# Kernel optimization log

Measured on AMD Instinct MI355X. Metric: run time of the kernel, lower is better.

## Reference

```python
import jax, jax.numpy as jnp
import numpy as np

D_STATE = 16
D_CONV = 4


def _diag_perm(H, W):
    perm = []
    for off in range(-(H - 1), W):
        for i in range(H):
            j = i + off
            if 0 <= j < W:
                perm.append(i * W + j)
    perm = np.asarray(perm, dtype=np.int32)
    inv = np.argsort(perm).astype(np.int32)
    return perm, inv


def _mamba_block(x, W_in, conv_w, W_xproj, W_dt, b_dt, A_log, W_outm):
    # x: [B, L, E]; shared-weight SimplifiedMambaBlock, expand=1 -> d_inner = E
    Bsz, L, E = x.shape
    d_inner = W_in.shape[1] // 2
    d_state = W_xproj.shape[1] // 2
    xz = x @ W_in                              # [B, L, 2*d_inner]
    xi, z = xz[..., :d_inner], xz[..., d_inner:]
    # causal depthwise conv1d (padding=d_conv-1, trimmed to L)
    xc = jax.lax.conv_general_dilated(
        xi.transpose(0, 2, 1), conv_w, window_strides=(1,),
        padding=[(conv_w.shape[-1] - 1, 0)], feature_group_count=d_inner,
        dimension_numbers=('NCH', 'OIH', 'NCH'))
    xc = jax.nn.silu(xc.transpose(0, 2, 1))    # [B, L, d_inner]
    dtbc = xc @ W_xproj                        # [B, L, 2*d_state]
    dt = jax.nn.softplus(dtbc[..., :d_state] @ W_dt + b_dt)  # [B, L, d_inner]
    Bc = dtbc[..., d_state:]                   # [B, L, d_state]
    A = -jnp.exp(A_log)                        # [d_inner, d_state]

    def step(h, inp):
        dt_t, B_t, x_t = inp                   # [B,d_inner], [B,d_state], [B,d_inner]
        h = h * jnp.exp(A[None] * dt_t[:, :, None]) + B_t[:, None, :] * x_t[:, :, None]
        return h, h.sum(-1)

    h0 = jnp.zeros((Bsz, d_inner, d_state), x.dtype)
    _, y = jax.lax.scan(step, h0, (dt.transpose(1, 0, 2), Bc.transpose(1, 0, 2), xc.transpose(1, 0, 2)))
    y = y.transpose(1, 0, 2)                   # [B, L, d_inner]
    return (y * jax.nn.silu(z)) @ W_outm


def setup_inputs() -> dict:
    key = jax.random.key(0)
    ks = jax.random.split(key, 16)
    B, H, W, E = 8, 32, 32, 1024
    d_inner, d_state = E, D_STATE
    s = lambda n: 1.0 / np.sqrt(n)
    A = np.tile(np.arange(1, d_state + 1, dtype=np.float32), (d_inner, 1))
    return {
        'vision_features': jax.random.normal(ks[0], (B, H * W, E), jnp.float32),
        'W_input': jax.random.normal(ks[1], (E, E), jnp.float32) * s(E),
        'W_in': jax.random.normal(ks[2], (E, 2 * d_inner), jnp.float32) * s(E),
        'conv_w': jax.random.normal(ks[3], (d_inner, 1, D_CONV), jnp.float32) * s(D_CONV),
        'W_xproj': jax.random.normal(ks[4], (d_inner, 2 * d_state), jnp.float32) * s(d_inner),
        'W_dt': jax.random.normal(ks[5], (d_state, d_inner), jnp.float32) * s(d_state),
        'b_dt': jax.random.normal(ks[6], (d_inner,), jnp.float32) * 0.01,
        'A_log': jnp.asarray(np.log(A)),
        'W_outm': jax.random.normal(ks[7], (d_inner, E), jnp.float32) * s(d_inner),
        'dir_w': jnp.full((4,), 0.25, jnp.float32),
        'ln_g': jnp.ones((E,), jnp.float32),
        'ln_b': jnp.zeros((E,), jnp.float32),
        'W_outproj': jax.random.normal(ks[8], (E, E), jnp.float32) * s(E),
        'Wg1': jax.random.normal(ks[9], (E, E // 4), jnp.float32) * s(E),
        'Wg2': jax.random.normal(ks[10], (E // 4, 1), jnp.float32) * s(E // 4),
        'height': H,
        'width': W,
    }


def reference(vision_features, W_input, W_in, conv_w, W_xproj, W_dt, b_dt, A_log,
              W_outm, dir_w, ln_g, ln_b, W_outproj, Wg1, Wg2, height, width):
    B, N, E = vision_features.shape
    H, Wd = int(height), int(width)
    mamba = lambda t: _mamba_block(t, W_in, conv_w, W_xproj, W_dt, b_dt, A_log, W_outm)
    x = vision_features @ W_input              # [B, N, E]
    x2d = x.reshape(B, H, Wd, E)
    # direction 1: row-major
    out1 = mamba(x)
    # direction 2: flipped both spatial dims
    xf = jnp.flip(x2d, (1, 2)).reshape(B, N, E)
    out2 = jnp.flip(mamba(xf).reshape(B, H, Wd, E), (1, 2)).reshape(B, N, E)
    # direction 3: column-major (transpose)
    xt = x2d.transpose(0, 2, 1, 3).reshape(B, N, E)
    out3 = mamba(xt).reshape(B, Wd, H, E).transpose(0, 2, 1, 3).reshape(B, N, E)
    # direction 4: anti-diagonal scan
    perm, inv = _diag_perm(H, Wd)
    out4 = mamba(x[:, perm])[:, inv]
    fused = dir_w[0] * out1 + dir_w[1] * out2 + dir_w[2] * out3 + dir_w[3] * out4
    mu = fused.mean(-1, keepdims=True)
    var = ((fused - mu) ** 2).mean(-1, keepdims=True)
    fused = (fused - mu) * jax.lax.rsqrt(var + 1e-5) * ln_g + ln_b
    enhanced = fused @ W_outproj
    g = jax.nn.sigmoid(jax.nn.silu(vision_features.mean(1, keepdims=True) @ Wg1) @ Wg2)  # [B,1,1]
    return vision_features + g * enhanced
```

## Files before the change

### kernel.cpp

```cpp
#include <hip/hip_runtime.h>

typedef unsigned short u16;
typedef unsigned int u32;
typedef short v8s __attribute__((ext_vector_type(8)));
typedef float v4f __attribute__((ext_vector_type(4)));
typedef float v2f __attribute__((ext_vector_type(2)));

#define B_SZ 8
#define HH 32
#define WW 32
#define NN 1024
#define M1 (B_SZ * NN)
#define M4 (4 * M1)
#define NCHUNK 16
#define CLEN 64
#define CTB 8

__device__ __forceinline__ float bf2f(u16 u) {
    u32 x = ((u32)u) << 16;
    return __builtin_bit_cast(float, x);
}
__device__ __forceinline__ u16 f2bf(float f) {
    u32 x = __builtin_bit_cast(u32, f);
    x = x + 0x7fffu + ((x >> 16) & 1u);
    return (u16)(x >> 16);
}
__device__ __forceinline__ float rcp_(float x) { return __builtin_amdgcn_rcpf(x); }
__device__ __forceinline__ float sigmoidf_(float x) { return rcp_(1.f + __expf(-x)); }
__device__ __forceinline__ float ldf(const void* p, size_t i, int fin) {
    return fin ? ((const float*)p)[i] : bf2f(((const u16*)p)[i]);
}
__device__ __forceinline__ u16 ldbf(const void* p, size_t i, int fin) {
    return fin ? f2bf(((const float*)p)[i]) : ((const u16*)p)[i];
}
__device__ __forceinline__ void gload_lds16(const u16* g, u16* l) {
    __builtin_amdgcn_global_load_lds(
        (const __attribute__((address_space(1))) unsigned int*)g,
        (__attribute__((address_space(3))) unsigned int*)l, 16, 0, 0);
}
__device__ __forceinline__ int dirmap(int d, int t, const int* __restrict__ perm3) {
    if (d == 0) return t;
    if (d == 1) return (NN - 1) - t;
    if (d == 2) return (t & (HH - 1)) * WW + (t >> 5);
    return perm3[t];
}

__global__ void setup_kernel(const u16* __restrict__ raw, int* __restrict__ flags,
                             int* __restrict__ perm, int* __restrict__ inv) {
    if (blockIdx.x == 0 && threadIdx.x == 0) {
        int ok = 0;
        for (int i = 0; i < 512; i++) {
            int e = (raw[i] >> 7) & 0xFF;
            ok += (e >= 100 && e <= 140) ? 1 : 0;
        }
        flags[0] = (ok < 460) ? 1 : 0;
    }
    int t = blockIdx.x * blockDim.x + threadIdx.x;
    if (t >= NN) return;
    int i = t / WW, j = t % WW;
    int off = j - i;
    int start = 0;
    for (int o = -(HH - 1); o < off; ++o) {
        int lo = (0 > -o) ? 0 : -o;
        int hi = (HH - 1 < WW - 1 - o) ? (HH - 1) : (WW - 1 - o);
        start += (hi - lo + 1);
    }
    int lo0 = (0 > -off) ? 0 : -off;
    int r = start + (i - lo0);
    perm[r] = t;
    inv[t] = r;
}

__global__ __launch_bounds__(256) void convert_bf(const void* __restrict__ src,
                                                  u16* __restrict__ dst,
                                                  const int* __restrict__ flags, int n) {
    int fin = flags[0];
    int i = blockIdx.x * 256 + threadIdx.x;
    if (i < n) dst[i] = ldbf(src, (size_t)i, fin);
}

__global__ __launch_bounds__(256) void zero_f32(float* __restrict__ p, int n) {
    int i = blockIdx.x * 256 + threadIdx.x;
    if (i < n) p[i] = 0.f;
}

__global__ __launch_bounds__(256) void transpose_pad4(
        const void* __restrict__ s0, u16* __restrict__ d0,
        const void* __restrict__ s1, u16* __restrict__ d1,
        const void* __restrict__ s2, u16* __restrict__ d2,
        const void* __restrict__ s3, u16* __restrict__ d3,
        const int* __restrict__ flags) {
    int fin = flags[0];
    const int K = 1024;
    int yb = blockIdx.y;
    const void* src;
    u16* dst;
    int Nsrc, n0;
    if (yb < 64)       { src = s0; dst = d0; Nsrc = 2048; n0 = yb * 32; }
    else if (yb < 66)  { src = s1; dst = d1; Nsrc = 32;   n0 = (yb - 64) * 32; }
    else if (yb < 98)  { src = s2; dst = d2; Nsrc = 1024; n0 = (yb - 66) * 32; }
    else               { src = s3; dst = d3; Nsrc = 1024; n0 = (yb - 98) * 32; }
    __shared__ u16 tile[32][33];
    int k0 = blockIdx.x * 32;
    int tx = threadIdx.x & 31, ty = threadIdx.x >> 5;
#pragma unroll
    for (int i = 0; i < 4; i++) {
        int k = k0 + ty + i * 8, n = n0 + tx;
        tile[ty + i * 8][tx] = (n < Nsrc) ? ldbf(src, (size_t)k * Nsrc + n, fin) : (u16)0;
    }
    __syncthreads();
#pragma unroll
    for (int i = 0; i < 4; i++) {
        int n = n0 + ty + i * 8, k = k0 + tx;
        dst[(size_t)n * K + k] = tile[tx][ty + i * 8];
    }
}

template <int EM, int WI, int WJ>
__global__ __launch_bounds__(256, 4) void gemm128(const u16* __restrict__ A,
                                                  const u16* __restrict__ Bt,
                                                  void* __restrict__ out0,
                                                  void* __restrict__ out1,
                                                  int M, int N, int K,
                                                  const int* __restrict__ flags,
                                                  const void* __restrict__ aux0,
                                                  const float* __restrict__ aux1) {
    constexpr int BM = WI * 32;
    constexpr int BN = WJ * 32;
    int fin = flags[0];
    __shared__ __align__(16) u16 As[BM][64];
    __shared__ __align__(16) u16 Bs[BN][64];
    int tid = threadIdx.x;
    int wave = tid >> 6, lane = tid & 63, quad = lane >> 4, l16 = lane & 15;
    int wm = wave >> 1, wn = wave & 1;
    int m0 = blockIdx.x * BM, n0 = blockIdx.y * BN;
    int r8 = tid >> 3, p8 = tid & 7;
    int sw = (p8 ^ (r8 & 7)) * 8;

    const u16* aBase = A  + (size_t)(m0 + r8) * K + sw;
    const u16* bBase = Bt + (size_t)(n0 + r8) * K + sw;
    size_t rstride = (size_t)32 * K;

    v4f acc[WI][WJ];
#pragma unroll
    for (int i = 0; i < WI; i++)
#pragma unroll
        for (int j = 0; j < WJ; j++) acc[i][j] = (v4f){0.f, 0.f, 0.f, 0.f};

    int seg0 = ((0 + quad) ^ (l16 & 7)) * 8;
    int seg1 = ((4 + quad) ^ (l16 & 7)) * 8;

    for (int k0 = 0; k0 < K; k0 += 64) {
#pragma unroll
        for (int c = 0; c < BM / 32; c++)
            gload_lds16(aBase + (size_t)c * rstride + k0, &As[c * 32 + r8][p8 * 8]);
#pragma unroll
        for (int c = 0; c < BN / 32; c++)
            gload_lds16(bBase + (size_t)c * rstride + k0, &Bs[c * 32 + r8][p8 * 8]);
        __syncthreads();
        v8s af[WI], bf[WJ];
#pragma unroll
        for (int i = 0; i < WI; i++)
            af[i] = *(const v8s*)&As[wm * (WI * 16) + i * 16 + l16][seg0];
#pragma unroll
        for (int j = 0; j < WJ; j++)
            bf[j] = *(const v8s*)&Bs[wn * (WJ * 16) + j * 16 + l16][seg0];
#pragma unroll
        for (int i = 0; i < WI; i++)
#pragma unroll
            for (int j = 0; j < WJ; j++)
                acc[i][j] = __builtin_amdgcn_mfma_f32_16x16x32_bf16(af[i], bf[j],
                                                                    acc[i][j], 0, 0, 0);
#pragma unroll
        for (int i = 0; i < WI; i++)
            af[i] = *(const v8s*)&As[wm * (WI * 16) + i * 16 + l16][seg1];
#pragma unroll
        for (int j = 0; j < WJ; j++)
            bf[j] = *(const v8s*)&Bs[wn * (WJ * 16) + j * 16 + l16][seg1];
#pragma unroll
        for (int i = 0; i < WI; i++)
#pragma unroll
            for (int j = 0; j < WJ; j++)
                acc[i][j] = __builtin_amdgcn_mfma_f32_16x16x32_bf16(af[i], bf[j],
                                                                    acc[i][j], 0, 0, 0);
        __syncthreads();
    }

#pragma unroll
    for (int i = 0; i < WI; i++) {
#pragma unroll
        for (int j = 0; j < WJ; j++) {
#pragma unroll
            for (int rr = 0; rr < 4; rr++) {
                int row = m0 + wm * (WI * 16) + i * 16 + quad * 4 + rr;
                int col = n0 + wn * (WJ * 16) + j * 16 + l16;
                float v = acc[i][j][rr];
                size_t oi = (size_t)row * N + col;
                if (EM == 0) {
                    ((u16*)out0)[oi] = f2bf(v);
                } else if (EM == 1) {
                    if (col < 1024) {
                        ((u16*)out0)[(size_t)row * 1024 + col] = f2bf(v);
                    } else {
                        float sz = v * sigmoidf_(v);
                        ((u16*)out1)[(size_t)row * 1024 + (col - 1024)] = f2bf(sz);
                    }
                } else if (EM == 5) {
                    ((float*)out0)[oi] = v;
                } else {
                    float g = aux1[row >> 10];
                    float res = ldf(aux0, oi, fin) + g * v;
                    if (fin) ((float*)out0)[oi] = res;
                    else ((u16*)out0)[oi] = f2bf(res);
                }
            }
        }
    }
}

__global__ __launch_bounds__(256) void conv_tile(const u16* __restrict__ xi,
                                                 const void* __restrict__ cw,
                                                 u16* __restrict__ xc4,
                                                 const int* __restrict__ flags,
                                                 const int* __restrict__ perm3) {
    int fin = flags[0];
    int gblk = blockIdx.x;
    int d = gblk >> 10, blk = gblk & 1023;
    int b = blk >> 7, tc = blk & 127;
    int t0 = tc * CTB;
    __shared__ u16 rows[CTB + 3][1024];
    __shared__ int sp[CTB + 3];
    if (threadIdx.x < CTB + 3) {
        int tt = t0 - 3 + (int)threadIdx.x;
        sp[threadIdx.x] = (tt >= 0) ? dirmap(d, tt, perm3) : -1;
    }
    __syncthreads();
    for (int i = threadIdx.x; i < (CTB + 3) * 128; i += 256) {
        int r = i >> 7, off = (i & 127) * 8;
        int src = sp[r];
        uint4 v = make_uint4(0, 0, 0, 0);
        if (src >= 0)
            v = *(const uint4*)(xi + ((size_t)(b * 1024 + src)) * 1024 + off);
        *(uint4*)&rows[r][off] = v;
    }
    int e0 = threadIdx.x * 4;
    float w[4][4];
#pragma unroll
    for (int ee = 0; ee < 4; ee++)
#pragma unroll
        for (int k = 0; k < 4; k++)
            w[ee][k] = ldf(cw, (size_t)(e0 + ee) * 4 + k, fin);
    __syncthreads();
    u16* outp = xc4 + (size_t)d * M1 * 1024;
#pragma unroll
    for (int t = 0; t < CTB; t++) {
        float a[4] = {0.f, 0.f, 0.f, 0.f};
#pragma unroll
        for (int k = 0; k < 4; k++) {
            uint2 v = *(const uint2*)&rows[t + k][e0];
            const u16* vs = (const u16*)&v;
#pragma unroll
            for (int ee = 0; ee < 4; ee++)
                a[ee] += w[ee][k] * bf2f(vs[ee]);
        }
        u16 o[4];
#pragma unroll
        for (int ee = 0; ee < 4; ee++) o[ee] = f2bf(a[ee] * sigmoidf_(a[ee]));
        *(uint2*)(outp + ((size_t)(b * 1024 + t0 + t)) * 1024 + e0) = *(const uint2*)o;
    }
}

#define SHUF_LO(q) __builtin_shufflevector(q, q, 0, 1)
#define SHUF_HI(q) __builtin_shufflevector(q, q, 2, 3)
#define SCAN_TLOOP(FASTV)                                                      \
    for (int t = 0; t < CLEN; t++) {                                           \
        float xn = 0.f, zn = 0.f;                                              \
        if (t + 1 < CLEN) {                                                    \
            xn = bf2f(xcyz[ix + 1024]);                                        \
            if (PASS == 3) zn = bf2f(zb[zbase + (size_t)s_perm[t + 1] * 1024]);\
        }                                                                      \
        v4f q0 = *(const v4f*)&sdt[t][0];                                      \
        v4f q1 = *(const v4f*)&sdt[t][4];                                      \
        v4f q2 = *(const v4f*)&sdt[t][8];                                      \
        v4f q3 = *(const v4f*)&sdt[t][12];                                     \
        v2f xpv = {bd, 0.f};                                                   \
        xpv += SHUF_LO(q0) * wdt2[0];                                          \
        xpv += SHUF_HI(q0) * wdt2[1];                                          \
        xpv += SHUF_LO(q1) * wdt2[2];                                          \
        xpv += SHUF_HI(q1) * wdt2[3];                                          \
        xpv += SHUF_LO(q2) * wdt2[4];                                          \
        xpv += SHUF_HI(q2) * wdt2[5];                                          \
        xpv += SHUF_LO(q3) * wdt2[6];                                          \
        xpv += SHUF_HI(q3) * wdt2[7];                                          \
        float xp = xpv.x + xpv.y;                                              \
        float ex = __expf(xp);                                                 \
        v4f r0 = *(const v4f*)&sdt[t][16];                                     \
        v4f r1 = *(const v4f*)&sdt[t][20];                                     \
        v4f r2 = *(const v4f*)&sdt[t][24];                                     \
        v4f r3 = *(const v4f*)&sdt[t][28];                                     \
        v2f bc[8];                                                             \
        bc[0] = SHUF_LO(r0); bc[1] = SHUF_HI(r0);                              \
        bc[2] = SHUF_LO(r1); bc[3] = SHUF_HI(r1);                              \
        bc[4] = SHUF_LO(r2); bc[5] = SHUF_HI(r2);                              \
        bc[6] = SHUF_LO(r3); bc[7] = SHUF_HI(r3);                              \
        v2f acc2 = {0.f, 0.f};                                                 \
        if (FASTV) {                                                           \
            float E = rcp_(1.f + ex);           \
            v2f Ev; Ev.x = E; Ev.y = E * E;                                    \
            v2f Estep; Estep.x = Ev.y; Estep.y = Ev.y;                         \
            _Pragma("unroll")                                                  \
            for (int p = 0; p < 8; p++) {                                      \
                h2[p] = h2[p] * Ev + bc[p] * xv;                               \
                acc2 += h2[p];                                                 \
                Ev *= Estep;                                                   \
            }                                                                  \
            if (PASS == 1) ds *= E;                   \
        } else {                                                               \
            float dtv = (xp > 15.f) ? xp : __logf(1.f + ex);                   \
            _Pragma("unroll")                                                  \
            for (int p = 0; p < 8; p++) {                                      \
                v2f es;                                                        \
                es.x = __expf(Ae2[p].x * dtv);                                 \
                es.y = __expf(Ae2[p].y * dtv);                                 \
                h2[p] = h2[p] * es + bc[p] * xv;                               \
                acc2 += h2[p];                                                 \
            }                                                                  \
            if (PASS == 1) ds += dtv;                                          \
        }                                                                      \
        if (PASS == 3) {                                                       \
            float accv = acc2.x + acc2.y;                                      \
            xcyz[ix] = f2bf(accv * zv * wd);  \
        }                                                                      \
        ix += 1024;                                                            \
        xv = xn;                                                               \
        zv = zn;                                                               \
    }

template <int PASS>
__global__ __launch_bounds__(256) void scan_chunk(const float* __restrict__ dtbc,
                                                  u16* __restrict__ xcyz,
                                                  const u16* __restrict__ zb,
                                                  const void* __restrict__ A_log,
                                                  const void* __restrict__ W_dt,
                                                  const void* __restrict__ b_dt,
                                                  const int* __restrict__ flags,
                                                  float* __restrict__ hend,
                                                  float* __restrict__ dtsum,
                                                  const void* __restrict__ dirw,
                                                  const int* __restrict__ perm3) {
    int fin = flags[0];
    int bid = blockIdx.x;
    int ec = bid & 3, c = (bid >> 2) & (NCHUNK - 1), b = (bid >> 6) & 7, d = bid >> 9;
    int e = ec * 256 + threadIdx.x;
    size_t row0 = (size_t)d * M1 + b * 1024 + c * CLEN;
    size_t cix  = (size_t)d * (8 * NCHUNK) + b * NCHUNK + c;
    __shared__ float sdt[CLEN][32];
    __shared__ int s_perm[CLEN];
    {
        const float* src = dtbc + row0 * 64;
        for (int i = threadIdx.x; i < CLEN * 8; i += 256) {
            int t = i >> 3, f = i & 7;
            *(float4*)&sdt[t][f * 4] = *(const float4*)(src + (size_t)t * 64 + f * 4);
        }
        if (PASS == 3 && threadIdx.x < CLEN)
            s_perm[threadIdx.x] = dirmap(d, c * CLEN + (int)threadIdx.x, perm3);
    }
    v2f Ae2[8], wdt2[8];
    bool fast = true;
#pragma unroll
    for (int p = 0; p < 8; p++) {
        float a0 = -__expf(ldf(A_log, (size_t)e * 16 + 2 * p, fin));
        float a1 = -__expf(ldf(A_log, (size_t)e * 16 + 2 * p + 1, fin));
        Ae2[p].x = a0;
        Ae2[p].y = a1;
        fast = fast && fabsf(a0 + (float)(2 * p + 1)) < 1e-3f * (2 * p + 1)
                    && fabsf(a1 + (float)(2 * p + 2)) < 1e-3f * (2 * p + 2);
    }
#pragma unroll
    for (int p = 0; p < 8; p++) {
        wdt2[p].x = ldf(W_dt, (size_t)(2 * p) * 1024 + e, fin);
        wdt2[p].y = ldf(W_dt, (size_t)(2 * p + 1) * 1024 + e, fin);
    }
    float bd = ldf(b_dt, e, fin);
    float wd = (PASS == 3) ? ldf(dirw, d, fin) : 0.f;
    v2f h2[8];
    if (PASS == 1) {
#pragma unroll
        for (int p = 0; p < 8; p++) h2[p] = (v2f){0.f, 0.f};
    } else {
#pragma unroll
        for (int p = 0; p < 8; p++) {
            h2[p].x = hend[(cix * 16 + 2 * p) * 1024 + e];
            h2[p].y = hend[(cix * 16 + 2 * p + 1) * 1024 + e];
        }
    }
    __syncthreads();
    float ds = fast ? 1.f : 0.f;
    size_t ix = row0 * 1024 + e;
    size_t zbase = (size_t)b * 1024 * 1024 + e;
    float xv = bf2f(xcyz[ix]);
    float zv = (PASS == 3) ? bf2f(zb[zbase + (size_t)s_perm[0] * 1024]) : 0.f;
    if (fast) {
        SCAN_TLOOP(true)
    } else {
        SCAN_TLOOP(false)
    }
    if (PASS == 1) {
#pragma unroll
        for (int p = 0; p < 8; p++) {
            hend[(cix * 16 + 2 * p) * 1024 + e] = h2[p].x;
            hend[(cix * 16 + 2 * p + 1) * 1024 + e] = h2[p].y;
        }
        dtsum[cix * 1024 + e] = ds;
    }
}

__global__ __launch_bounds__(256) void scan_combine2(float* __restrict__ hend,
                                                     const float* __restrict__ dtsum,
                                                     const void* __restrict__ A_log,
                                                     const int* __restrict__ flags) {
    int fin = flags[0];
    int bid = blockIdx.x;
    int ec = bid & 3, s = (bid >> 2) & 15, b = (bid >> 6) & 7, d = bid >> 9;
    int e = ec * 256 + threadIdx.x;
    bool fast = true;
#pragma unroll
    for (int s2 = 0; s2 < 16; s2++) {
        float a = -__expf(ldf(A_log, (size_t)e * 16 + s2, fin));
        fast = fast && fabsf(a + (float)(s2 + 1)) < 1e-3f * (s2 + 1);
    }
    float Ae = -__expf(ldf(A_log, (size_t)e * 16 + s, fin));
    float H = 0.f;
    size_t base = (size_t)d * (8 * NCHUNK) + (size_t)b * NCHUNK;
    for (int c = 0; c < NCHUNK; c++) {
        size_t cix = base + c;
        float ds = dtsum[cix * 1024 + e];
        float decay;
        if (fast) {
            float r = 1.f, bb = ds;
            int n = s + 1;
            while (n) {
                if (n & 1) r *= bb;
                bb *= bb;
                n >>= 1;
            }
            decay = r;
        } else {
            decay = __expf(Ae * ds);
        }
        size_t idx = (cix * 16 + s) * 1024 + e;
        float loc = hend[idx];
        hend[idx] = H;
        H = loc + decay * H;
    }
}

__global__ __launch_bounds__(256) void ln4_kernel(const u16* __restrict__ y4,
                                                  const void* __restrict__ ln_g,
                                                  const void* __restrict__ ln_b,
                                                  const int* __restrict__ flags,
                                                  const int* __restrict__ inv3,
                                                  u16* __restrict__ fn) {
    int fin = flags[0];
    int row = blockIdx.x;
    int b = row >> 10, q = row & 1023;
    int t1 = 1023 - q;
    int t2 = ((q & 31) << 5) | (q >> 5);
    int t3 = inv3[q];
    const u16* p0 = y4 + ((size_t)(b * 1024 + q)) * 1024;
    const u16* p1 = y4 + ((size_t)(M1 + b * 1024 + t1)) * 1024;
    const u16* p2 = y4 + ((size_t)(2 * M1 + b * 1024 + t2)) * 1024;
    const u16* p3 = y4 + ((size_t)(3 * M1 + b * 1024 + t3)) * 1024;
    int e0 = threadIdx.x * 4;
    uint2 a0 = *(const uint2*)(p0 + e0);
    uint2 a1 = *(const uint2*)(p1 + e0);
    uint2 a2 = *(const uint2*)(p2 + e0);
    uint2 a3 = *(const uint2*)(p3 + e0);
    const u16* s0 = (const u16*)&a0;
    const u16* s1 = (const u16*)&a1;
    const u16* s2 = (const u16*)&a2;
    const u16* s3 = (const u16*)&a3;
    float v[4];
    float sum = 0.f, sq = 0.f;
#pragma unroll
    for (int j = 0; j < 4; j++) {
        float f = bf2f(s0[j]) + bf2f(s1[j]) + bf2f(s2[j]) + bf2f(s3[j]);
        v[j] = f;
        sum += f;
        sq += f * f;
    }
    __shared__ float r1[256], r2[256];
    r1[threadIdx.x] = sum;
    r2[threadIdx.x] = sq;
    __syncthreads();
    for (int s = 128; s > 0; s >>= 1) {
        if (threadIdx.x < s) {
            r1[threadIdx.x] += r1[threadIdx.x + s];
            r2[threadIdx.x] += r2[threadIdx.x + s];
        }
        __syncthreads();
    }
    float mu = r1[0] * (1.f / 1024.f);
    float var = r2[0] * (1.f / 1024.f) - mu * mu;
    float rs = rsqrtf(var + 1e-5f);
    u16 o[4];
#pragma unroll
    for (int j = 0; j < 4; j++) {
        int e = e0 + j;
        o[j] = f2bf((v[j] - mu) * rs * ldf(ln_g, e, fin) + ldf(ln_b, e, fin));
    }
    *(uint2*)(fn + (size_t)row * 1024 + e0) = *(const uint2*)o;
}

__global__ __launch_bounds__(256) void gate_partial(const u16* __restrict__ vfb,
                                                    float* __restrict__ meanv) {
    int b = blockIdx.x >> 4, tc = blockIdx.x & 15;
    float s[4] = {0.f, 0.f, 0.f, 0.f};
    const u16* base = vfb + ((size_t)b * 1024 + tc * 64) * 1024;
    for (int t = 0; t < 64; t++) {
#pragma unroll
        for (int k = 0; k < 4; k++)
            s[k] += bf2f(base[(size_t)t * 1024 + threadIdx.x + k * 256]);
    }
#pragma unroll
    for (int k = 0; k < 4; k++)
        atomicAdd(&meanv[b * 1024 + threadIdx.x + k * 256], s[k]);
}

__global__ __launch_bounds__(256) void gate_mv(const float* __restrict__ meanv,
                                               const void* __restrict__ Wg1,
                                               const int* __restrict__ flags,
                                               float* __restrict__ gpart) {
    int fin = flags[0];
    int kc = blockIdx.x, j = threadIdx.x;
    __shared__ float mv[8][32];
    if (threadIdx.x < 8 * 32) {
        int b = threadIdx.x >> 5, kk = threadIdx.x & 31;
        mv[b][kk] = meanv[b * 1024 + kc * 32 + kk] * (1.f / 1024.f);
    }
    __syncthreads();
    float acc[8];
#pragma unroll
    for (int b = 0; b < 8; b++) acc[b] = 0.f;
    for (int kk = 0; kk < 32; kk++) {
        float w = ldf(Wg1, (size_t)(kc * 32 + kk) * 256 + j, fin);
#pragma unroll
        for (int b = 0; b < 8; b++) acc[b] += mv[b][kk] * w;
    }
#pragma unroll
    for (int b = 0; b < 8; b++) atomicAdd(&gpart[b * 256 + j], acc[b]);
}

__global__ __launch_bounds__(256) void gate_fin2(const float* __restrict__ gpart,
                                                 const void* __restrict__ Wg2,
                                                 const int* __restrict__ flags,
                                                 float* __restrict__ g) {
    int fin = flags[0];
    int b = blockIdx.x, j = threadIdx.x;
    __shared__ float red[256];
    float a = gpart[b * 256 + j];
    float si = a * sigmoidf_(a);
    red[j] = si * ldf(Wg2, j, fin);
    __syncthreads();
    for (int st = 128; st > 0; st >>= 1) {
        if (j < st) red[j] += red[j + st];
        __syncthreads();
    }
    if (j == 0) g[b] = sigmoidf_(red[0]);
}

extern "C" void kernel_launch(void* const* d_in, const int* in_sizes, int n_in,
                              void* d_out, int out_size, void* d_ws, size_t ws_size,
                              hipStream_t stream) {
    const void* vf_raw  = d_in[0];
    const void* W_input = d_in[1];
    const void* W_in    = d_in[2];
    const void* conv_w  = d_in[3];
    const void* W_xproj = d_in[4];
    const void* W_dt    = d_in[5];
    const void* b_dt    = d_in[6];
    const void* A_log   = d_in[7];
    const void* W_outm  = d_in[8];
    const void* dir_w   = d_in[9];
    const void* ln_g    = d_in[10];
    const void* ln_b    = d_in[11];
    const void* W_outpj = d_in[12];
    const void* Wg1     = d_in[13];
    const void* Wg2     = d_in[14];

    char* ws = (char*)d_ws;
    size_t off = 0;
    auto alloc = [&](size_t bytes) -> void* {
        void* p = ws + off;
        off = (off + bytes + 255) & ~(size_t)255;
        return p;
    };
    int*   flags = (int*)alloc(256);
    int*   perm3 = (int*)alloc(NN * 4);
    int*   inv3  = (int*)alloc(NN * 4);
    float* meanv = (float*)alloc(8 * 1024 * 4);
    float* gpart = (float*)alloc(8 * 256 * 4);
    float* gbuf  = (float*)alloc(64);
    u16*   WiB   = (u16*)alloc((size_t)1024 * 1024 * 2);
    u16*   WtIn  = (u16*)alloc((size_t)2048 * 1024 * 2);
    u16*   WtF   = (u16*)alloc((size_t)2048 * 1024 * 2);
    u16*   WtXp  = (u16*)alloc((size_t)64 * 1024 * 2);
    u16*   WtOm  = (u16*)alloc((size_t)1024 * 1024 * 2);
    u16*   WtOp  = (u16*)alloc((size_t)1024 * 1024 * 2);
    u16*   vfb   = (u16*)alloc((size_t)M1 * 1024 * 2);
    u16*   xbuf  = (u16*)alloc((size_t)M1 * 1024 * 2);
    float* tail32= (float*)alloc((size_t)M1 * 1024 * 4);
    u16*   xi    = (u16*)alloc((size_t)M1 * 1024 * 2);
    u16*   zb    = (u16*)alloc((size_t)M1 * 1024 * 2);
    u16*   xc4   = (u16*)alloc((size_t)M4 * 1024 * 2);
    float* dtbc4 = (float*)alloc((size_t)M4 * 64 * 4);
    float* dtsum4= (float*)alloc((size_t)4 * 8 * NCHUNK * 1024 * 4);
    float* hend4 = (float*)vfb;
    u16*   y4    = (u16*)vfb;
    (void)tail32;
    (void)xbuf;

    setup_kernel<<<4, 256, 0, stream>>>((const u16*)vf_raw, flags, perm3, inv3);
    convert_bf<<<(M1 * 1024) / 256, 256, 0, stream>>>(vf_raw, vfb, flags, M1 * 1024);
    convert_bf<<<(1024 * 1024) / 256, 256, 0, stream>>>(W_input, WiB, flags, 1024 * 1024);
    transpose_pad4<<<dim3(32, 130), 256, 0, stream>>>(
        W_in, WtIn, W_xproj, WtXp, W_outm, WtOm, W_outpj, WtOp, flags);
    zero_f32<<<40, 256, 0, stream>>>(meanv, 8 * 1024 + 8 * 256);

    gemm128<0, 2, 2><<<dim3(32, 16), 256, 0, stream>>>(
        WtIn, WiB, WtF, nullptr, 2048, 1024, 1024, flags, nullptr, nullptr);

    gate_partial<<<128, 256, 0, stream>>>(vfb, meanv);
    gate_mv<<<32, 256, 0, stream>>>(meanv, Wg1, flags, gpart);
    gate_fin2<<<8, 256, 0, stream>>>(gpart, Wg2, flags, gbuf);

    gemm128<1, 4, 4><<<dim3(64, 16), 256, 0, stream>>>(
        vfb, WtF, xi, zb, M1, 2048, 1024, flags, nullptr, nullptr);

    conv_tile<<<4096, 256, 0, stream>>>(xi, conv_w, xc4, flags, perm3);
    gemm128<5, 2, 2><<<dim3(512, 1), 256, 0, stream>>>(
        xc4, WtXp, dtbc4, nullptr, M4, 64, 1024, flags, nullptr, nullptr);
    scan_chunk<1><<<2048, 256, 0, stream>>>(dtbc4, xc4, zb, A_log, W_dt, b_dt,
                                            flags, hend4, dtsum4, dir_w, perm3);
    scan_combine2<<<2048, 256, 0, stream>>>(hend4, dtsum4, A_log, flags);
    scan_chunk<3><<<2048, 256, 0, stream>>>(dtbc4, xc4, zb, A_log, W_dt, b_dt,
                                            flags, hend4, dtsum4, dir_w, perm3);

    gemm128<0, 4, 4><<<dim3(256, 8), 256, 0, stream>>>(
        xc4, WtOm, y4, nullptr, M4, 1024, 1024, flags, nullptr, nullptr);

    u16* fn = xi;
    ln4_kernel<<<M1, 256, 0, stream>>>(y4, ln_g, ln_b, flags, inv3, fn);
    gemm128<4, 4, 4><<<dim3(64, 8), 256, 0, stream>>>(
        fn, WtOp, d_out, nullptr, M1, 1024, 1024, flags, vf_raw, gbuf);
}
```

Baseline: 615.9 us.

## Process two channels per thread in chunked scan to amortize shared dt/B loads

Each scan_chunk thread now handles two adjacent d_inner channels, reusing the per-timestep shared-memory dt/B reads for both and using packed 32-bit global loads and stores for x, z and y. The grid is halved to match, and launch bounds request 4 blocks per SM. The slow path reloads A_log through volatile loads inside the inner loop to save registers, which would be expensive if that path ran. Doubling per-thread state raises register pressure and halves the number of parallel threads.

```diff
diff --git a/kernel.cpp b/kernel.cpp
--- a/kernel.cpp
+++ b/kernel.cpp
@@ -29,6 +29,10 @@
 __device__ __forceinline__ float sigmoidf_(float x) { return rcp_(1.f + __expf(-x)); }
 __device__ __forceinline__ float ldf(const void* p, size_t i, int fin) {
     return fin ? ((const float*)p)[i] : bf2f(((const u16*)p)[i]);
+}
+__device__ __forceinline__ float ldf_v(const void* p, size_t i, int fin) {
+    return fin ? ((volatile const float*)p)[i]
+               : bf2f(((volatile const u16*)p)[i]);
 }
 __device__ __forceinline__ u16 ldbf(const void* p, size_t i, int fin) {
     return fin ? f2bf(((const float*)p)[i]) : ((const u16*)p)[i];
@@ -274,26 +278,29 @@
 #define SHUF_HI(q) __builtin_shufflevector(q, q, 2, 3)
 #define SCAN_TLOOP(FASTV)                                                      \
     for (int t = 0; t < CLEN; t++) {                                           \
-        float xn = 0.f, zn = 0.f;                                              \
+        u32 xnw = 0, znw = 0;                                                  \
         if (t + 1 < CLEN) {                                                    \
-            xn = bf2f(xcyz[ix + 1024]);                                        \
-            if (PASS == 3) zn = bf2f(zb[zbase + (size_t)s_perm[t + 1] * 1024]);\
+            xnw = *(const u32*)&xcyz[ix + 1024];                               \
+            if (PASS == 3)                                                     \
+                znw = *(const u32*)&zb[zbase + (size_t)s_perm[t + 1] * 1024];  \
         }                                                                      \
         v4f q0 = *(const v4f*)&sdt[t][0];                                      \
         v4f q1 = *(const v4f*)&sdt[t][4];                                      \
         v4f q2 = *(const v4f*)&sdt[t][8];                                      \
         v4f q3 = *(const v4f*)&sdt[t][12];                                     \
-        v2f xpv = {bd, 0.f};                                                   \
-        xpv += SHUF_LO(q0) * wdt2[0];                                          \
-        xpv += SHUF_HI(q0) * wdt2[1];                                          \
-        xpv += SHUF_LO(q1) * wdt2[2];                                          \
-        xpv += SHUF_HI(q1) * wdt2[3];                                          \
-        xpv += SHUF_LO(q2) * wdt2[4];                                          \
-        xpv += SHUF_HI(q2) * wdt2[5];                                          \
-        xpv += SHUF_LO(q3) * wdt2[6];                                          \
-        xpv += SHUF_HI(q3) * wdt2[7];                                          \
-        float xp = xpv.x + xpv.y;                                              \
-        float ex = __expf(xp);                                                 \
+        v2f xpvA = {bdA, 0.f}, xpvB = {bdB, 0.f};                              \
+        xpvA += SHUF_LO(q0) * wdtA[0]; xpvB += SHUF_LO(q0) * wdtB[0];          \
+        xpvA += SHUF_HI(q0) * wdtA[1]; xpvB += SHUF_HI(q0) * wdtB[1];          \
+        xpvA += SHUF_LO(q1) * wdtA[2]; xpvB += SHUF_LO(q1) * wdtB[2];          \
+        xpvA += SHUF_HI(q1) * wdtA[3]; xpvB += SHUF_HI(q1) * wdtB[3];          \
+        xpvA += SHUF_LO(q2) * wdtA[4]; xpvB += SHUF_LO(q2) * wdtB[4];          \
+        xpvA += SHUF_HI(q2) * wdtA[5]; xpvB += SHUF_HI(q2) * wdtB[5];          \
+        xpvA += SHUF_LO(q3) * wdtA[6]; xpvB += SHUF_LO(q3) * wdtB[6];          \
+        xpvA += SHUF_HI(q3) * wdtA[7]; xpvB += SHUF_HI(q3) * wdtB[7];          \
+        float xpA = xpvA.x + xpvA.y;                                           \
+        float xpB = xpvB.x + xpvB.y;                                           \
+        float exA = __expf(xpA);                                               \
+        float exB = __expf(xpB);                                               \
         v4f r0 = *(const v4f*)&sdt[t][16];                                     \
         v4f r1 = *(const v4f*)&sdt[t][20];                                     \
         v4f r2 = *(const v4f*)&sdt[t][24];                                     \
@@ -303,55 +310,72 @@
         bc[2] = SHUF_LO(r1); bc[3] = SHUF_HI(r1);                              \
         bc[4] = SHUF_LO(r2); bc[5] = SHUF_HI(r2);                              \
         bc[6] = SHUF_LO(r3); bc[7] = SHUF_HI(r3);                              \
-        v2f acc2 = {0.f, 0.f};                                                 \
+        v2f accA = {0.f, 0.f}, accB = {0.f, 0.f};                              \
         if (FASTV) {                                                           \
-            float E = rcp_(1.f + ex);           \
-            v2f Ev; Ev.x = E; Ev.y = E * E;                                    \
-            v2f Estep; Estep.x = Ev.y; Estep.y = Ev.y;                         \
+            float EA = rcp_(1.f + exA);                                        \
+            float EB = rcp_(1.f + exB);                                        \
+            v2f EvA; EvA.x = EA; EvA.y = EA * EA;                              \
+            v2f EvB; EvB.x = EB; EvB.y = EB * EB;                              \
+            v2f EsA; EsA.x = EvA.y; EsA.y = EvA.y;                             \
+            v2f EsB; EsB.x = EvB.y; EsB.y = EvB.y;                             \
             _Pragma("unroll")                                                  \
             for (int p = 0; p < 8; p++) {                                      \
-                h2[p] = h2[p] * Ev + bc[p] * xv;                               \
-                acc2 += h2[p];                                                 \
-                Ev *= Estep;                                                   \
+                hA[p] = hA[p] * EvA + bc[p] * xvA;                             \
+                hB[p] = hB[p] * EvB + bc[p] * xvB;                             \
+                accA += hA[p];                                                 \
+                accB += hB[p];                                                 \
+                EvA *= EsA;                                                    \
+                EvB *= EsB;                                                    \
             }                                                                  \
-            if (PASS == 1) ds *= E;                   \
+            if (PASS == 1) { dsA *= EA; dsB *= EB; }                           \
         } else {                                                               \
-            float dtv = (xp > 15.f) ? xp : __logf(1.f + ex);                   \
+            float dtvA = (xpA > 15.f) ? xpA : __logf(1.f + exA);               \
+            float dtvB = (xpB > 15.f) ? xpB : __logf(1.f + exB);               \
             _Pragma("unroll")                                                  \
             for (int p = 0; p < 8; p++) {                                      \
-                v2f es;                                                        \
-                es.x = __expf(Ae2[p].x * dtv);                                 \
-                es.y = __expf(Ae2[p].y * dtv);                                 \
-                h2[p] = h2[p] * es + bc[p] * xv;                               \
-                acc2 += h2[p];                                                 \
+                v2f esA, esB;                                                  \
+                esA.x = __expf(-__expf(ldf_v(A_log, (size_t)e0 * 16 + 2 * p, fin)) * dtvA); \
+                esA.y = __expf(-__expf(ldf_v(A_log, (size_t)e0 * 16 + 2 * p + 1, fin)) * dtvA); \
+                esB.x = __expf(-__expf(ldf_v(A_log, (size_t)(e0 + 1) * 16 + 2 * p, fin)) * dtvB); \
+                esB.y = __expf(-__expf(ldf_v(A_log, (size_t)(e0 + 1) * 16 + 2 * p + 1, fin)) * dtvB); \
+                hA[p] = hA[p] * esA + bc[p] * xvA;                             \
+                hB[p] = hB[p] * esB + bc[p] * xvB;                             \
+                accA += hA[p];                                                 \
+                accB += hB[p];                                                 \
             }                                                                  \
-            if (PASS == 1) ds += dtv;                                          \
+            if (PASS == 1) { dsA += dtvA; dsB += dtvB; }                       \
         }                                                                      \
         if (PASS == 3) {                                                       \
-            float accv = acc2.x + acc2.y;                                      \
-            xcyz[ix] = f2bf(accv * zv * wd);  \
+            float oA = (accA.x + accA.y) * zvA * wd;                           \
+            float oB = (accB.x + accB.y) * zvB * wd;                           \
+            u32 ow = (u32)f2bf(oA) | ((u32)f2bf(oB) << 16);                    \
+            *(u32*)&xcyz[ix] = ow;                                             \
         }                                                                      \
         ix += 1024;                                                            \
-        xv = xn;                                                               \
-        zv = zn;                                                               \
+        xvA = bf2f((u16)(xnw & 0xffff));                                       \
+        xvB = bf2f((u16)(xnw >> 16));                                          \
+        if (PASS == 3) {                                                       \
+            zvA = bf2f((u16)(znw & 0xffff));                                   \
+            zvB = bf2f((u16)(znw >> 16));                                      \
+        }                                                                      \
     }
 
 template <int PASS>
-__global__ __launch_bounds__(256) void scan_chunk(const float* __restrict__ dtbc,
-                                                  u16* __restrict__ xcyz,
-                                                  const u16* __restrict__ zb,
-                                                  const void* __restrict__ A_log,
-                                                  const void* __restrict__ W_dt,
-                                                  const void* __restrict__ b_dt,
-                                                  const int* __restrict__ flags,
-                                                  float* __restrict__ hend,
-                                                  float* __restrict__ dtsum,
-                                                  const void* __restrict__ dirw,
-                                                  const int* __restrict__ perm3) {
+__global__ __launch_bounds__(256, 4) void scan_chunk(const float* __restrict__ dtbc,
+                                                     u16* __restrict__ xcyz,
+                                                     const u16* __restrict__ zb,
+                                                     const void* __restrict__ A_log,
+                                                     const void* __restrict__ W_dt,
+                                                     const void* __restrict__ b_dt,
+                                                     const int* __restrict__ flags,
+                                                     float* __restrict__ hend,
+                                                     float* __restrict__ dtsum,
+                                                     const void* __restrict__ dirw,
+                                                     const int* __restrict__ perm3) {
     int fin = flags[0];
     int bid = blockIdx.x;
-    int ec = bid & 3, c = (bid >> 2) & (NCHUNK - 1), b = (bid >> 6) & 7, d = bid >> 9;
-    int e = ec * 256 + threadIdx.x;
+    int ec = bid & 1, c = (bid >> 1) & (NCHUNK - 1), b = (bid >> 5) & 7, d = bid >> 8;
+    int e0 = ec * 512 + (int)threadIdx.x * 2;
     size_t row0 = (size_t)d * M1 + b * 1024 + c * CLEN;
     size_t cix  = (size_t)d * (8 * NCHUNK) + b * NCHUNK + c;
     __shared__ float sdt[CLEN][32];
@@ -365,41 +389,59 @@
         if (PASS == 3 && threadIdx.x < CLEN)
             s_perm[threadIdx.x] = dirmap(d, c * CLEN + (int)threadIdx.x, perm3);
     }
-    v2f Ae2[8], wdt2[8];
     bool fast = true;
 #pragma unroll
     for (int p = 0; p < 8; p++) {
-        float a0 = -__expf(ldf(A_log, (size_t)e * 16 + 2 * p, fin));
-        float a1 = -__expf(ldf(A_log, (size_t)e * 16 + 2 * p + 1, fin));
-        Ae2[p].x = a0;
-        Ae2[p].y = a1;
+        float a0 = -__expf(ldf(A_log, (size_t)e0 * 16 + 2 * p, fin));
+        float a1 = -__expf(ldf(A_log, (size_t)e0 * 16 + 2 * p + 1, fin));
+        float b0 = -__expf(ldf(A_log, (size_t)(e0 + 1) * 16 + 2 * p, fin));
+        float b1 = -__expf(ldf(A_log, (size_t)(e0 + 1) * 16 + 2 * p + 1, fin));
         fast = fast && fabsf(a0 + (float)(2 * p + 1)) < 1e-3f * (2 * p + 1)
-                    && fabsf(a1 + (float)(2 * p + 2)) < 1e-3f * (2 * p + 2);
-    }
+                    && fabsf(a1 + (float)(2 * p + 2)) < 1e-3f * (2 * p + 2)
+                    && fabsf(b0 + (float)(2 * p + 1)) < 1e-3f * (2 * p + 1)
+                    && fabsf(b1 + (float)(2 * p + 2)) < 1e-3f * (2 * p + 2);
+    }
+    v2f wdtA[8], wdtB[8];
 #pragma unroll
     for (int p = 0; p < 8; p++) {
-        wdt2[p].x = ldf(W_dt, (size_t)(2 * p) * 1024 + e, fin);
-        wdt2[p].y = ldf(W_dt, (size_t)(2 * p + 1) * 1024 + e, fin);
-    }
-    float bd = ldf(b_dt, e, fin);
+        wdtA[p].x = ldf(W_dt, (size_t)(2 * p) * 1024 + e0, fin);
+        wdtA[p].y = ldf(W_dt, (size_t)(2 * p + 1) * 1024 + e0, fin);
+        wdtB[p].x = ldf(W_dt, (size_t)(2 * p) * 1024 + e0 + 1, fin);
+        wdtB[p].y = ldf(W_dt, (size_t)(2 * p + 1) * 1024 + e0 + 1, fin);
+    }
+    float bdA = ldf(b_dt, e0, fin);
+    float bdB = ldf(b_dt, e0 + 1, fin);
     float wd = (PASS == 3) ? ldf(dirw, d, fin) : 0.f;
-    v2f h2[8];
+    v2f hA[8], hB[8];
     if (PASS == 1) {
 #pragma unroll
-        for (int p = 0; p < 8; p++) h2[p] = (v2f){0.f, 0.f};
+        for (int p = 0; p < 8; p++) {
+            hA[p] = (v2f){0.f, 0.f};
+            hB[p] = (v2f){0.f, 0.f};
+        }
     } else {
 #pragma unroll
         for (int p = 0; p < 8; p++) {
-            h2[p].x = hend[(cix * 16 + 2 * p) * 1024 + e];
-            h2[p].y = hend[(cix * 16 + 2 * p + 1) * 1024 + e];
+            v2f lo_ = *(const v2f*)&hend[(cix * 16 + 2 * p) * 1024 + e0];
+            v2f hi_ = *(const v2f*)&hend[(cix * 16 + 2 * p + 1) * 1024 + e0];
+            hA[p] = (v2f){lo_.x, hi_.x};
+            hB[p] = (v2f){lo_.y, hi_.y};
         }
     }
     __syncthreads();
-    float ds = fast ? 1.f : 0.f;
-    size_t ix = row0 * 1024 + e;
-    size_t zbase = (size_t)b * 1024 * 1024 + e;
-    float xv = bf2f(xcyz[ix]);
-    float zv = (PASS == 3) ? bf2f(zb[zbase + (size_t)s_perm[0] * 1024]) : 0.f;
+    float dsA = fast ? 1.f : 0.f;
+    float dsB = dsA;
+    size_t ix = row0 * 1024 + e0;
+    size_t zbase = (size_t)b * 1024 * 1024 + e0;
+    u32 xw0 = *(const u32*)&xcyz[ix];
+    float xvA = bf2f((u16)(xw0 & 0xffff));
+    float xvB = bf2f((u16)(xw0 >> 16));
+    float zvA = 0.f, zvB = 0.f;
+    if (PASS == 3) {
+        u32 zw0 = *(const u32*)&zb[zbase + (size_t)s_perm[0] * 1024];
+        zvA = bf2f((u16)(zw0 & 0xffff));
+        zvB = bf2f((u16)(zw0 >> 16));
+    }
     if (fast) {
         SCAN_TLOOP(true)
     } else {
@@ -408,10 +450,10 @@
     if (PASS == 1) {
 #pragma unroll
         for (int p = 0; p < 8; p++) {
-            hend[(cix * 16 + 2 * p) * 1024 + e] = h2[p].x;
-            hend[(cix * 16 + 2 * p + 1) * 1024 + e] = h2[p].y;
-        }
-        dtsum[cix * 1024 + e] = ds;
+            *(v2f*)&hend[(cix * 16 + 2 * p) * 1024 + e0] = (v2f){hA[p].x, hB[p].x};
+            *(v2f*)&hend[(cix * 16 + 2 * p + 1) * 1024 + e0] = (v2f){hA[p].y, hB[p].y};
+        }
+        *(v2f*)&dtsum[cix * 1024 + e0] = (v2f){dsA, dsB};
     }
 }
 
@@ -640,10 +682,10 @@
     conv_tile<<<4096, 256, 0, stream>>>(xi, conv_w, xc4, flags, perm3);
     gemm128<5, 2, 2><<<dim3(512, 1), 256, 0, stream>>>(
         xc4, WtXp, dtbc4, nullptr, M4, 64, 1024, flags, nullptr, nullptr);
-    scan_chunk<1><<<2048, 256, 0, stream>>>(dtbc4, xc4, zb, A_log, W_dt, b_dt,
+    scan_chunk<1><<<1024, 256, 0, stream>>>(dtbc4, xc4, zb, A_log, W_dt, b_dt,
                                             flags, hend4, dtsum4, dir_w, perm3);
     scan_combine2<<<2048, 256, 0, stream>>>(hend4, dtsum4, A_log, flags);
-    scan_chunk<3><<<2048, 256, 0, stream>>>(dtbc4, xc4, zb, A_log, W_dt, b_dt,
+    scan_chunk<3><<<1024, 256, 0, stream>>>(dtbc4, xc4, zb, A_log, W_dt, b_dt,
                                             flags, hend4, dtsum4, dir_w, perm3);
 
     gemm128<0, 4, 4><<<dim3(256, 8), 256, 0, stream>>>(
```

Result: no change. 625.3 us (+1.5%).
